# Kernel tuning notes

Hardware: AMD Instinct MI355X
Metric: run time of the kernel (lower is better)

The kernel has to match this reference:

```python
import jax, jax.numpy as jnp
import numpy as np

NODE_FEATURES = 256
HIDDEN = 32
N_NODES = 100000
N_EDGES = 3200000


def _glorot(key, shape):
    fan_in, fan_out = shape[-2], shape[-1]
    lim = (6.0 / (fan_in + fan_out)) ** 0.5
    return jax.random.uniform(key, shape, jnp.float32, -lim, lim)


def setup_inputs() -> dict:
    key = jax.random.key(0)
    ks = jax.random.split(key, 12)
    in_cat = NODE_FEATURES + HIDDEN  # DConv input is cat([X, H])
    x = jax.random.normal(ks[0], (N_NODES, NODE_FEATURES), jnp.float32)
    edge_index = jax.random.randint(ks[1], (2, N_EDGES), 0, N_NODES, jnp.int64)
    return {
        "x": x,
        "edge_index": edge_index,
        # DConv weights have shape (2, K=1, in, out); squeeze K -> (2, in, out)
        "w_z": _glorot(ks[2], (2, in_cat, HIDDEN)),
        "b_z": jnp.zeros((HIDDEN,), jnp.float32),
        "w_r": _glorot(ks[3], (2, in_cat, HIDDEN)),
        "b_r": jnp.zeros((HIDDEN,), jnp.float32),
        "w_h": _glorot(ks[4], (2, in_cat, HIDDEN)),
        "b_h": jnp.zeros((HIDDEN,), jnp.float32),
        # fc head, stored as [in, out]
        "fc1_w": _glorot(ks[5], (HIDDEN, HIDDEN)),
        "fc1_b": jnp.zeros((HIDDEN,), jnp.float32),
        "fc2_w": _glorot(ks[6], (HIDDEN, 1)),
        "fc2_b": jnp.zeros((1,), jnp.float32),
    }


def _dconv_k1(inp, w, b):
    # K=1 DConv: only the k=0 Chebyshev term for both diffusion directions,
    # i.e. no propagation over edges. H = X @ W_out + X @ W_in + bias.
    return inp @ (w[0] + w[1]) + b


def reference(x, edge_index, w_z, b_z, w_r, b_r, w_h, b_h, fc1_w, fc1_b, fc2_w, fc2_b):
    n = x.shape[0]
    h0 = jnp.zeros((n, HIDDEN), x.dtype)  # DCRNN called with H=None -> zeros
    xh0 = jnp.concatenate([x, h0], axis=1)  # [N, F+H]
    z = jax.nn.sigmoid(_dconv_k1(xh0, w_z, b_z))  # update gate
    r = jax.nn.sigmoid(_dconv_k1(xh0, w_r, b_r))  # reset gate
    xrh = jnp.concatenate([x, r * h0], axis=1)
    h_tilde = jnp.tanh(_dconv_k1(xrh, w_h, b_h))
    h = z * h0 + (1.0 - z) * h_tilde  # [N, 32]
    # fc head: Linear-ReLU-Dropout(eval=identity)-Linear-Sigmoid
    hidden = jax.nn.relu(h @ fc1_w + fc1_b)
    out = jax.nn.sigmoid(hidden @ fc2_w + fc2_b)  # [N, 1]
    return out
```

## Files before the change

kernel.cpp:

```cpp
#include <hip/hip_runtime.h>
#include <hip/hip_bf16.h>


#define NF     256
#define NOUT   64
#define MB     128
#define NTHR   256
#define KCHUNK 128
#define XSTR   132
#define HPAD   36

typedef __attribute__((ext_vector_type(8)))  short  short8;
typedef __attribute__((ext_vector_type(16))) float  floatx16;

__device__ __forceinline__ unsigned f2bf(float f) {
    __hip_bfloat16 h = __float2bfloat16(f);
    return (unsigned)*(unsigned short*)&h;
}
__device__ __forceinline__ float fast_sigmoid(float v) {
    return 1.0f / (1.0f + __expf(-v));
}
__device__ __forceinline__ float fast_tanh(float v) {
    return 1.0f - 2.0f / (1.0f + __expf(2.0f * v));
}

__global__ void prep_W(const float* __restrict__ wz,
                       const float* __restrict__ wh,
                       unsigned short* __restrict__ Wf)
{
    int idx = blockIdx.x * blockDim.x + threadIdx.x;
    if (idx >= NF * NOUT) return;
    int j    = idx & 7;
    int lane = (idx >> 3) & 63;
    int nt   = (idx >> 9) & 1;
    int kt   = idx >> 10;
    int k = kt * 16 + (lane >> 5) * 8 + j;
    int o = nt * 32 + (lane & 31);
    const int PLANE = 288 * 32;
    float v;
    if (o < 32) v = wz[k * 32 + o]        + wz[PLANE + k * 32 + o];
    else        v = wh[k * 32 + (o - 32)] + wh[PLANE + k * 32 + (o - 32)];
    Wf[idx] = (unsigned short)f2bf(v);
}

__global__ void __launch_bounds__(NTHR, 4)
rgcn_main(const float* __restrict__ x,
          const unsigned short* __restrict__ Wf,
          const float* __restrict__ bz,
          const float* __restrict__ bh,
          const float* __restrict__ fc1w,
          const float* __restrict__ fc1b,
          const float* __restrict__ fc2w,
          const float* __restrict__ fc2b,
          float* __restrict__ out,
          int n_nodes)
{
    __shared__ __align__(16) char S[MB * XSTR * 2];
    unsigned short* Xb = (unsigned short*)S;
    float* Hs = (float*)S;
    float* Ps = (float*)(S + MB * HPAD * 4);

    const int tid   = threadIdx.x;
    const int lane  = tid & 63;
    const int wave  = tid >> 6;
    const int wb    = wave * 32;
    const int node0 = blockIdx.x * MB;

    floatx16 acc0 = {};
    floatx16 acc1 = {};

    for (int c = 0; c < 2; ++c) {
        __syncthreads();
#pragma unroll
        for (int i = 0; i < 16; ++i) {
            int nn   = (tid >> 5) + i * 8;
            int slot = tid & 31;
            float4 v = make_float4(0.f, 0.f, 0.f, 0.f);
            int gn = node0 + nn;
            if (gn < n_nodes)
                v = *(const float4*)(x + (size_t)gn * NF + c * KCHUNK + slot * 4);
            unsigned lo = f2bf(v.x) | (f2bf(v.y) << 16);
            unsigned hi = f2bf(v.z) | (f2bf(v.w) << 16);
            *(uint2*)(Xb + nn * XSTR + slot * 4) = make_uint2(lo, hi);
        }
        __syncthreads();

#pragma unroll
        for (int kt = 0; kt < 8; ++kt) {
            int ktg = c * 8 + kt;
            const uint4* bp = (const uint4*)Wf + (size_t)(ktg * 2) * 64 + lane;
            uint4 b0u = bp[0];
            uint4 b1u = bp[64];
            const unsigned short* ap =
                Xb + (wb + (lane & 31)) * XSTR + kt * 16 + (lane >> 5) * 8;
            uint2 alo = *(const uint2*)(ap);
            uint2 ahi = *(const uint2*)(ap + 4);
            union { short8 s; uint2 u[2]; } a, b0, b1;
            a.u[0] = alo; a.u[1] = ahi;
            b0.u[0] = make_uint2(b0u.x, b0u.y); b0.u[1] = make_uint2(b0u.z, b0u.w);
            b1.u[0] = make_uint2(b1u.x, b1u.y); b1.u[1] = make_uint2(b1u.z, b1u.w);
            acc0 = __builtin_amdgcn_mfma_f32_32x32x16_bf16(a.s, b0.s, acc0, 0, 0, 0);
            acc1 = __builtin_amdgcn_mfma_f32_32x32x16_bf16(a.s, b1.s, acc1, 0, 0, 0);
        }
    }

    const int nc   = lane & 31;
    const float bzn = bz[nc];
    const float bhn = bh[nc];
    __syncthreads();
#pragma unroll
    for (int r = 0; r < 16; ++r) {
        int row = (r & 3) + 8 * (r >> 2) + 4 * (lane >> 5);
        float z = fast_sigmoid(acc0[r] + bzn);
        float t = fast_tanh   (acc1[r] + bhn);
        Hs[(wb + row) * HPAD + nc] = (1.0f - z) * t;
    }
    __syncthreads();

    const int nl   = tid & (MB - 1);
    const int half = tid >> 7;
    float h[32];
#pragma unroll
    for (int m = 0; m < 8; ++m) {
        float4 v = *(const float4*)(Hs + nl * HPAD + m * 4);
        h[m * 4 + 0] = v.x; h[m * 4 + 1] = v.y;
        h[m * 4 + 2] = v.z; h[m * 4 + 3] = v.w;
    }
    float part = 0.0f;
    for (int jj = 0; jj < 16; ++jj) {
        int j = half * 16 + jj;
        float s = fc1b[j];
#pragma unroll
        for (int o = 0; o < 32; ++o)
            s = fmaf(h[o], fc1w[o * 32 + j], s);
        part = fmaf(fmaxf(s, 0.0f), fc2w[j], part);
    }
    if (half == 1) Ps[nl] = part;
    __syncthreads();
    if (half == 0) {
        int gn = node0 + nl;
        if (gn < n_nodes)
            out[gn] = fast_sigmoid(part + Ps[nl] + fc2b[0]);
    }
}

extern "C" void kernel_launch(void* const* d_in, const int* in_sizes, int n_in,
                              void* d_out, int out_size, void* d_ws, size_t ws_size,
                              hipStream_t stream) {
    const float* x    = (const float*)d_in[0];
    const float* wz   = (const float*)d_in[2];
    const float* bz   = (const float*)d_in[3];
    const float* wh   = (const float*)d_in[6];
    const float* bh   = (const float*)d_in[7];
    const float* fc1w = (const float*)d_in[8];
    const float* fc1b = (const float*)d_in[9];
    const float* fc2w = (const float*)d_in[10];
    const float* fc2b = (const float*)d_in[11];
    float* out = (float*)d_out;
    unsigned short* Wf = (unsigned short*)d_ws;

    const int n = in_sizes[0] / NF;

    prep_W<<<(NF * NOUT + 255) / 256, 256, 0, stream>>>(wz, wh, Wf);
    rgcn_main<<<(n + MB - 1) / MB, NTHR, 0, stream>>>(
        x, Wf, bz, bh, fc1w, fc1b, fc2w, fc2b, out, n);
}
```

Before: 206.6 us.

## Load x directly into MFMA A-fragments and make waves independent of LDS staging

Removes the shared-memory staging of x. Each lane now reads its own node row from global memory, converts it to bf16 and feeds the MFMA directly, so each wave owns a 32-node tile. The cross-half reduction in the fc head uses a wave shuffle instead of LDS plus a block barrier, and launch bounds drop from 4 to 3 blocks per SM. This avoids LDS writes and reads and two barriers per K chunk. In exchange, global loads become strided per lane (32 bytes per row per step), which may coalesce less well than the old row-contiguous loads.

```diff
diff --git a/kernel.cpp b/kernel.cpp
--- a/kernel.cpp
+++ b/kernel.cpp
@@ -2,13 +2,12 @@
 #include <hip/hip_bf16.h>
 
 
-#define NF     256
-#define NOUT   64
-#define MB     128
-#define NTHR   256
-#define KCHUNK 128
-#define XSTR   132
-#define HPAD   36
+#define NF    256
+#define TILE  32
+#define WPB   4
+#define MB    (TILE * WPB)
+#define NTHR  256
+#define HSTR  36
 
 typedef __attribute__((ext_vector_type(8)))  short  short8;
 typedef __attribute__((ext_vector_type(16))) float  floatx16;
@@ -29,7 +28,7 @@
                        unsigned short* __restrict__ Wf)
 {
     int idx = blockIdx.x * blockDim.x + threadIdx.x;
-    if (idx >= NF * NOUT) return;
+    if (idx >= NF * 64) return;
     int j    = idx & 7;
     int lane = (idx >> 3) & 63;
     int nt   = (idx >> 9) & 1;
@@ -43,7 +42,7 @@
     Wf[idx] = (unsigned short)f2bf(v);
 }
 
-__global__ void __launch_bounds__(NTHR, 4)
+__global__ void __launch_bounds__(NTHR, 3)
 rgcn_main(const float* __restrict__ x,
           const unsigned short* __restrict__ Wf,
           const float* __restrict__ bz,
@@ -55,92 +54,77 @@
           float* __restrict__ out,
           int n_nodes)
 {
-    __shared__ __align__(16) char S[MB * XSTR * 2];
-    unsigned short* Xb = (unsigned short*)S;
-    float* Hs = (float*)S;
-    float* Ps = (float*)(S + MB * HPAD * 4);
+    __shared__ float Hs[WPB * TILE * HSTR];
 
     const int tid   = threadIdx.x;
     const int lane  = tid & 63;
     const int wave  = tid >> 6;
-    const int wb    = wave * 32;
-    const int node0 = blockIdx.x * MB;
+    const int node0 = blockIdx.x * MB + wave * TILE;
+
+    const int m    = lane & 31;
+    const int koff = (lane >> 5) * 8;
+    int gn_a = node0 + m;
+    if (gn_a >= n_nodes) gn_a = n_nodes - 1;
+    const float* xr = x + (size_t)gn_a * NF + koff;
 
     floatx16 acc0 = {};
     floatx16 acc1 = {};
 
-    for (int c = 0; c < 2; ++c) {
-        __syncthreads();
 #pragma unroll
-        for (int i = 0; i < 16; ++i) {
-            int nn   = (tid >> 5) + i * 8;
-            int slot = tid & 31;
-            float4 v = make_float4(0.f, 0.f, 0.f, 0.f);
-            int gn = node0 + nn;
-            if (gn < n_nodes)
-                v = *(const float4*)(x + (size_t)gn * NF + c * KCHUNK + slot * 4);
-            unsigned lo = f2bf(v.x) | (f2bf(v.y) << 16);
-            unsigned hi = f2bf(v.z) | (f2bf(v.w) << 16);
-            *(uint2*)(Xb + nn * XSTR + slot * 4) = make_uint2(lo, hi);
-        }
-        __syncthreads();
-
-#pragma unroll
-        for (int kt = 0; kt < 8; ++kt) {
-            int ktg = c * 8 + kt;
-            const uint4* bp = (const uint4*)Wf + (size_t)(ktg * 2) * 64 + lane;
-            uint4 b0u = bp[0];
-            uint4 b1u = bp[64];
-            const unsigned short* ap =
-                Xb + (wb + (lane & 31)) * XSTR + kt * 16 + (lane >> 5) * 8;
-            uint2 alo = *(const uint2*)(ap);
-            uint2 ahi = *(const uint2*)(ap + 4);
-            union { short8 s; uint2 u[2]; } a, b0, b1;
-            a.u[0] = alo; a.u[1] = ahi;
-            b0.u[0] = make_uint2(b0u.x, b0u.y); b0.u[1] = make_uint2(b0u.z, b0u.w);
-            b1.u[0] = make_uint2(b1u.x, b1u.y); b1.u[1] = make_uint2(b1u.z, b1u.w);
-            acc0 = __builtin_amdgcn_mfma_f32_32x32x16_bf16(a.s, b0.s, acc0, 0, 0, 0);
-            acc1 = __builtin_amdgcn_mfma_f32_32x32x16_bf16(a.s, b1.s, acc1, 0, 0, 0);
-        }
+    for (int kt = 0; kt < 16; ++kt) {
+        float4 v0 = *(const float4*)(xr + kt * 16);
+        float4 v1 = *(const float4*)(xr + kt * 16 + 4);
+        const uint4* bp = (const uint4*)Wf + (size_t)(kt * 2) * 64 + lane;
+        uint4 b0u = bp[0];
+        uint4 b1u = bp[64];
+        union { short8 s; unsigned u[4]; } a, b0, b1;
+        a.u[0] = f2bf(v0.x) | (f2bf(v0.y) << 16);
+        a.u[1] = f2bf(v0.z) | (f2bf(v0.w) << 16);
+        a.u[2] = f2bf(v1.x) | (f2bf(v1.y) << 16);
+        a.u[3] = f2bf(v1.z) | (f2bf(v1.w) << 16);
+        b0.u[0] = b0u.x; b0.u[1] = b0u.y; b0.u[2] = b0u.z; b0.u[3] = b0u.w;
+        b1.u[0] = b1u.x; b1.u[1] = b1u.y; b1.u[2] = b1u.z; b1.u[3] = b1u.w;
+        acc0 = __builtin_amdgcn_mfma_f32_32x32x16_bf16(a.s, b0.s, acc0, 0, 0, 0);
+        acc1 = __builtin_amdgcn_mfma_f32_32x32x16_bf16(a.s, b1.s, acc1, 0, 0, 0);
     }
 
-    const int nc   = lane & 31;
+    const int nc = lane & 31;
     const float bzn = bz[nc];
     const float bhn = bh[nc];
-    __syncthreads();
+    float* Hw = Hs + wave * TILE * HSTR;
 #pragma unroll
     for (int r = 0; r < 16; ++r) {
         int row = (r & 3) + 8 * (r >> 2) + 4 * (lane >> 5);
         float z = fast_sigmoid(acc0[r] + bzn);
         float t = fast_tanh   (acc1[r] + bhn);
-        Hs[(wb + row) * HPAD + nc] = (1.0f - z) * t;
+        Hw[row * HSTR + nc] = (1.0f - z) * t;
     }
     __syncthreads();
 
-    const int nl   = tid & (MB - 1);
-    const int half = tid >> 7;
+    const int nl   = lane & 31;
+    const int half = lane >> 5;
+    const float* hp = Hw + nl * HSTR;
     float h[32];
 #pragma unroll
-    for (int m = 0; m < 8; ++m) {
-        float4 v = *(const float4*)(Hs + nl * HPAD + m * 4);
-        h[m * 4 + 0] = v.x; h[m * 4 + 1] = v.y;
-        h[m * 4 + 2] = v.z; h[m * 4 + 3] = v.w;
+    for (int q = 0; q < 8; ++q) {
+        float4 v = *(const float4*)(hp + q * 4);
+        h[q * 4 + 0] = v.x; h[q * 4 + 1] = v.y;
+        h[q * 4 + 2] = v.z; h[q * 4 + 3] = v.w;
     }
     float part = 0.0f;
     for (int jj = 0; jj < 16; ++jj) {
-        int j = half * 16 + jj;
+        int j = (half << 4) + jj;
         float s = fc1b[j];
 #pragma unroll
         for (int o = 0; o < 32; ++o)
             s = fmaf(h[o], fc1w[o * 32 + j], s);
         part = fmaf(fmaxf(s, 0.0f), fc2w[j], part);
     }
-    if (half == 1) Ps[nl] = part;
-    __syncthreads();
+    part += __shfl_xor(part, 32);
     if (half == 0) {
         int gn = node0 + nl;
         if (gn < n_nodes)
-            out[gn] = fast_sigmoid(part + Ps[nl] + fc2b[0]);
+            out[gn] = fast_sigmoid(part + fc2b[0]);
     }
 }
 
@@ -161,7 +145,7 @@
 
     const int n = in_sizes[0] / NF;
 
-    prep_W<<<(NF * NOUT + 255) / 256, 256, 0, stream>>>(wz, wh, Wf);
+    prep_W<<<(NF * 64 + 255) / 256, 256, 0, stream>>>(wz, wh, Wf);
     rgcn_main<<<(n + MB - 1) / MB, NTHR, 0, stream>>>(
         x, Wf, bz, bh, fc1w, fc1b, fc2w, fc2b, out, n);
 }
```

Measured after the change: 209.5 us. No clear change (+1.4%).
